# Kernel tuning notes

Measured on AMD Instinct MI355X. Metric: run time of the kernel, lower is better.

## Reference

```python
import jax, jax.numpy as jnp
import numpy as np
import math

N, B, E = 1024, 1, 1024
H = 16
D = E // H
S = 128  # num_samples per row

def setup_inputs() -> dict:
    key = jax.random.key(0)
    ks = jax.random.split(key, 12)
    w = lambda k: jax.random.normal(k, (E, E), jnp.float32) * 0.02
    inp = {
        'query': jax.random.normal(ks[0], (N, B, E), jnp.float32),
        'key':   jax.random.normal(ks[1], (N, B, E), jnp.float32),
        'value': jax.random.normal(ks[2], (N, B, E), jnp.float32),
        'Wq': w(ks[3]), 'bq': jnp.zeros((E,), jnp.float32),
        'Wk': w(ks[4]), 'bk': jnp.zeros((E,), jnp.float32),
        'Wv': w(ks[5]), 'bv': jnp.zeros((E,), jnp.float32),
        'Wo': w(ks[6]), 'bo': jnp.zeros((E,), jnp.float32),
        # per-row sampled column indices, already offset+clamped to [0, N)
        'samples': jax.random.randint(ks[7], (N, S), 0, N, jnp.int32),
    }
    return inp

def reference(query, key, value, Wq, bq, Wk, bk, Wv, bv, Wo, bo, samples):
    n = query.shape[0]
    # projections (torch Linear: x @ W.T + b), split heads -> [B*H, n, D]
    q = (query @ Wq.T + bq).reshape(n, B * H, D).transpose(1, 0, 2)
    k = (key   @ Wk.T + bk).reshape(n, B * H, D).transpose(1, 0, 2)
    v = (value @ Wv.T + bv).reshape(n, B * H, D).transpose(1, 0, 2)
    # emulate per-row unique(): sort, mask duplicates (first occurrence kept)
    cols = jnp.sort(samples, axis=1)                              # [n, S]
    dup = jnp.concatenate([jnp.zeros((n, 1), bool), cols[:, 1:] == cols[:, :-1]], axis=1)
    kg = k[:, cols]                                               # [BH, n, S, D]
    scores = jnp.einsum('hid,hisd->his', q, kg) / jnp.float32(math.sqrt(n))
    scores = jnp.where(dup[None], jnp.float32(-1e30), scores)
    w = jax.nn.softmax(scores, axis=-1)                           # [BH, n, S]
    vg = v[:, cols]                                               # [BH, n, S, D]
    o = jnp.einsum('his,hisd->hid', w, vg)                        # [BH, n, D]
    o = o.transpose(1, 0, 2).reshape(n, B, E)
    return o @ Wo.T + bo
```

## Files before the change

### kernel.cpp

```cpp
#include <hip/hip_runtime.h>
#include <hip/hip_bf16.h>

#define NTOK 1024
#define EMB  1024
#define NH   16
#define HD   64
#define NS   128

typedef unsigned short u16;
typedef unsigned int uint;
typedef __attribute__((ext_vector_type(8))) unsigned short ushort8v;
typedef __attribute__((ext_vector_type(8))) _Float16 half8v;
typedef __attribute__((ext_vector_type(4))) float f32x4;

__device__ __forceinline__ u16 f2h_bits(float f) {
  union { _Float16 h; u16 u; } x; x.h = (_Float16)f; return x.u;
}

__device__ __forceinline__ void gload16(const u16* g, u16* l) {
  __builtin_amdgcn_global_load_lds(
      (const __attribute__((address_space(1))) uint*)g,
      (__attribute__((address_space(3))) uint*)l, 16, 0, 0);
}

__global__ __launch_bounds__(256) void cvt_mask(const float* __restrict__ S0,
                                                const float* __restrict__ S1,
                                                const float* __restrict__ S2,
                                                const float* __restrict__ S3,
                                                const float* __restrict__ S4,
                                                const float* __restrict__ S5,
                                                const float* __restrict__ S6,
                                                const int* __restrict__ samples,
                                                u16* __restrict__ D,
                                                uint* __restrict__ maskg) {
  const int z = blockIdx.y;
  const int t = threadIdx.x;
  if (z == 7) {
    __shared__ uint m[32];
    const int i = blockIdx.x;
    if (t < 32) m[t] = 0u;
    __syncthreads();
    if (t < NS) {
      const int c = samples[(size_t)i * NS + t];
      atomicOr(&m[c >> 5], 1u << (c & 31));
    }
    __syncthreads();
    if (t < 32) maskg[(size_t)i * 32 + t] = m[t];
    return;
  }
  const float* S;
  switch (z) {
    case 0: S = S0; break;
    case 1: S = S1; break;
    case 2: S = S2; break;
    case 3: S = S3; break;
    case 4: S = S4; break;
    case 5: S = S5; break;
    default: S = S6; break;
  }
  const int idx = blockIdx.x * 256 + t;
  const float4 f = ((const float4*)S)[idx];
  ushort4 p;
  p.x = f2h_bits(f.x); p.y = f2h_bits(f.y);
  p.z = f2h_bits(f.z); p.w = f2h_bits(f.w);
  ((ushort4*)(D + ((size_t)z << 20)))[idx] = p;
}

template<bool OUT_F16>
__global__ __launch_bounds__(256) void gemm3(const u16* __restrict__ Ab,
                                             const u16* __restrict__ Bb,
                                             const float* __restrict__ b0,
                                             const float* __restrict__ b1,
                                             const float* __restrict__ b2,
                                             void* __restrict__ Cp) {
  __shared__ u16 buf[2][2][64 * 32];

  const int t = threadIdx.x;
  const int lane = t & 63;
  const int w = t >> 6;
  const int wr = w >> 1, wc = w & 1;
  const int m0 = blockIdx.y * 64;
  const int n0 = blockIdx.x * 64;
  const int z = blockIdx.z;

  const u16* Az = Ab + ((size_t)z << 20);
  const u16* Bz = Bb + ((size_t)z << 20);
  const float* bsel = (z == 0) ? b0 : ((z == 1) ? b1 : b2);

  const int r_abs = w * 16 + (lane >> 2);
  const int schunk = (lane & 3) ^ ((r_abs >> 1) & 3);
  const u16* gA = Az + (size_t)(m0 + r_abs) * 1024 + schunk * 8;
  const u16* gB = Bz + (size_t)(n0 + r_abs) * 1024 + schunk * 8;
  u16* ldsA[2] = { &buf[0][0][(w * 16) * 32], &buf[1][0][(w * 16) * 32] };
  u16* ldsB[2] = { &buf[0][1][(w * 16) * 32], &buf[1][1][(w * 16) * 32] };

  const int fr = lane & 15;
  const int fq = lane >> 4;
  int offA[2], offB[2];
#pragma unroll
  for (int m = 0; m < 2; m++) {
    const int R = wr * 32 + m * 16 + fr;
    offA[m] = R * 32 + (fq ^ ((R >> 1) & 3)) * 8;
  }
#pragma unroll
  for (int n = 0; n < 2; n++) {
    const int R = wc * 32 + n * 16 + fr;
    offB[n] = R * 32 + (fq ^ ((R >> 1) & 3)) * 8;
  }

  f32x4 acc[2][2];
#pragma unroll
  for (int m = 0; m < 2; m++)
#pragma unroll
    for (int n = 0; n < 2; n++) acc[m][n] = (f32x4){0.f, 0.f, 0.f, 0.f};

  gload16(gA, ldsA[0]);
  gload16(gB, ldsB[0]);

  for (int kt = 0; kt < 32; kt++) {
    const int db = kt & 1;
    if (kt < 31) {
      const int k1 = (kt + 1) * 32;
      gload16(gA + k1, ldsA[db ^ 1]);
      gload16(gB + k1, ldsB[db ^ 1]);
      asm volatile("s_waitcnt vmcnt(2)" ::: "memory");
    } else {
      asm volatile("s_waitcnt vmcnt(0)" ::: "memory");
    }
    __builtin_amdgcn_s_barrier();
    __builtin_amdgcn_sched_barrier(0);

    const u16* cA = &buf[db][0][0];
    const u16* cB = &buf[db][1][0];
    half8v a0 = *(const half8v*)&cA[offA[0]];
    half8v a1 = *(const half8v*)&cA[offA[1]];
    half8v bv0 = *(const half8v*)&cB[offB[0]];
    half8v bv1 = *(const half8v*)&cB[offB[1]];
    acc[0][0] = __builtin_amdgcn_mfma_f32_16x16x32_f16(a0, bv0, acc[0][0], 0, 0, 0);
    acc[0][1] = __builtin_amdgcn_mfma_f32_16x16x32_f16(a0, bv1, acc[0][1], 0, 0, 0);
    acc[1][0] = __builtin_amdgcn_mfma_f32_16x16x32_f16(a1, bv0, acc[1][0], 0, 0, 0);
    acc[1][1] = __builtin_amdgcn_mfma_f32_16x16x32_f16(a1, bv1, acc[1][1], 0, 0, 0);

    asm volatile("s_waitcnt lgkmcnt(0)" ::: "memory");
    __builtin_amdgcn_s_barrier();
    __builtin_amdgcn_sched_barrier(0);
  }

  u16*   Cb = (u16*)Cp   + ((size_t)z << 20);
  float* Cf = (float*)Cp + ((size_t)z << 20);

  if (OUT_F16 && z == 2) {
#pragma unroll
    for (int n = 0; n < 2; n++) {
      const int col = n0 + wc * 32 + n * 16 + fr;
      const float bn = bsel[col];
#pragma unroll
      for (int m = 0; m < 2; m++) {
        const int rbase = m0 + wr * 32 + m * 16 + fq * 4;
        ushort4 pk;
        pk.x = f2h_bits(acc[m][n][0] + bn);
        pk.y = f2h_bits(acc[m][n][1] + bn);
        pk.z = f2h_bits(acc[m][n][2] + bn);
        pk.w = f2h_bits(acc[m][n][3] + bn);
        *(ushort4*)&Cb[(size_t)col * 1024 + rbase] = pk;
      }
    }
    return;
  }

#pragma unroll
  for (int n = 0; n < 2; n++) {
    const int col = n0 + wc * 32 + n * 16 + fr;
    const float bn = bsel[col];
#pragma unroll
    for (int m = 0; m < 2; m++) {
      const int rbase = m0 + wr * 32 + m * 16 + fq * 4;
#pragma unroll
      for (int r = 0; r < 4; r++) {
        const float val = acc[m][n][r] + bn;
        if constexpr (OUT_F16)
          Cb[(size_t)(rbase + r) * 1024 + col] = f2h_bits(val);
        else
          Cf[(size_t)(rbase + r) * 1024 + col] = val;
      }
    }
  }
}

__global__ __launch_bounds__(256) void attn7(const u16* __restrict__ Qh,
                                             const u16* __restrict__ Kh,
                                             const u16* __restrict__ Vtg,
                                             const uint* __restrict__ maskg,
                                             u16* __restrict__ O) {
  const int h  = blockIdx.x;
  const int qt = blockIdx.y;
  const int t  = threadIdx.x;
  const int wid = t >> 6;
  const int lane = t & 63;
  const int fr = lane & 15, fq = lane >> 4;

  __shared__ u16 Kl[2][128 * 64];
  __shared__ u16 Vl[2][64 * 128];
  __shared__ u16 Ps[4][16][136];
  __shared__ uint Ms[64][32];

  {
    const uint4* src = (const uint4*)(maskg + (size_t)qt * 64 * 32);
    uint4* dst = (uint4*)Ms;
    dst[t * 2]     = src[t * 2];
    dst[t * 2 + 1] = src[t * 2 + 1];
  }

  half8v qa0, qa1;
  {
    const u16* qp = Qh + (size_t)(qt * 64 + wid * 16 + fr) * EMB + h * HD + fq * 8;
    qa0 = *(const half8v*)qp;
    qa1 = *(const half8v*)(qp + 32);
  }

  const int kRow = wid * 32 + (lane >> 3);
  const int kChO = ((lane & 7) ^ ((lane >> 3) & 7)) * 8;
  const u16* kBase = Kh + h * HD + kChO;
  const int vSub = lane >> 4;
  const int vCh  = lane & 15;
  const u16* vBase = Vtg + (size_t)h * HD * NTOK;

  auto STAGE = [&](int kt_, int b_) {
#pragma unroll
    for (int ii = 0; ii < 4; ii++) {
      const int row = kRow + ii * 8;
      gload16(kBase + (size_t)(kt_ * 128 + row) * EMB,
              &Kl[b_][(wid * 32 + ii * 8) * 64]);
    }
#pragma unroll
    for (int ii = 0; ii < 4; ii++) {
      const int d = wid * 16 + ii * 4 + vSub;
      const int ch = (vCh ^ (d & 15)) * 8;
      gload16(vBase + (size_t)d * NTOK + kt_ * 128 + ch,
              &Vl[b_][(wid * 16 + ii * 4) * 128]);
    }
  };

  f32x4 oacc[4];
#pragma unroll
  for (int ds = 0; ds < 4; ds++) oacc[ds] = (f32x4){0.f, 0.f, 0.f, 0.f};
  float lsum[4] = {0.f, 0.f, 0.f, 0.f};

  STAGE(0, 0);

  for (int kt = 0; kt < 8; kt++) {
    if (kt < 7) {
      STAGE(kt + 1, (kt + 1) & 1);
      asm volatile("s_waitcnt vmcnt(8)" ::: "memory");
    } else {
      asm volatile("s_waitcnt vmcnt(0)" ::: "memory");
    }
    asm volatile("s_waitcnt lgkmcnt(0)" ::: "memory");
    __builtin_amdgcn_s_barrier();
    __builtin_amdgcn_sched_barrier(0);

    const u16* Kc = &Kl[kt & 1][0];
    const u16* Vc = &Vl[kt & 1][0];

    uint4 mq[4];
#pragma unroll
    for (int r = 0; r < 4; r++)
      mq[r] = *(const uint4*)&Ms[wid * 16 + fq * 4 + r][kt * 4];

#pragma unroll
    for (int jb = 0; jb < 8; jb++) {
      f32x4 s = (f32x4){0.f, 0.f, 0.f, 0.f};
      const int R = jb * 16 + fr;
      const half8v b0 = *(const half8v*)&Kc[R * 64 + (fq ^ (fr & 7)) * 8];
      const half8v b1 = *(const half8v*)&Kc[R * 64 + ((4 + fq) ^ (fr & 7)) * 8];
      s = __builtin_amdgcn_mfma_f32_16x16x32_f16(qa0, b0, s, 0, 0, 0);
      s = __builtin_amdgcn_mfma_f32_16x16x32_f16(qa1, b1, s, 0, 0, 0);
#pragma unroll
      for (int r = 0; r < 4; r++) {
        const uint mw = (jb >> 1) == 0 ? mq[r].x
                      : (jb >> 1) == 1 ? mq[r].y
                      : (jb >> 1) == 2 ? mq[r].z : mq[r].w;
        const float p = ((mw >> ((jb & 1) * 16 + fr)) & 1u)
                            ? __expf(s[r] * 0.03125f) : 0.f;
        lsum[r] += p;
        Ps[wid][fq * 4 + r][jb * 16 + fr] = f2h_bits(p);
      }
    }
    asm volatile("s_waitcnt lgkmcnt(0)" ::: "memory");
    __builtin_amdgcn_sched_barrier(0);

#pragma unroll
    for (int jc = 0; jc < 4; jc++) {
      const half8v pa = *(const half8v*)&Ps[wid][fr][jc * 32 + fq * 8];
#pragma unroll
      for (int ds = 0; ds < 4; ds++) {
        const int d = ds * 16 + fr;
        const half8v vb = *(const half8v*)&Vc[d * 128 + ((jc * 4 + fq) ^ fr) * 8];
        oacc[ds] = __builtin_amdgcn_mfma_f32_16x16x32_f16(pa, vb, oacc[ds], 0, 0, 0);
      }
    }
    __builtin_amdgcn_s_barrier();
  }

#pragma unroll
  for (int r = 0; r < 4; r++) {
    float v = lsum[r];
#pragma unroll
    for (int off = 1; off < 16; off <<= 1) v += __shfl_xor(v, off, 16);
    lsum[r] = v;
  }

#pragma unroll
  for (int ds = 0; ds < 4; ds++) {
#pragma unroll
    for (int r = 0; r < 4; r++) {
      O[(size_t)(qt * 64 + wid * 16 + fq * 4 + r) * EMB + h * HD + ds * 16 + fr] =
          f2h_bits(oacc[ds][r] / lsum[r]);
    }
  }
}

extern "C" void kernel_launch(void* const* d_in, const int* in_sizes, int n_in,
                              void* d_out, int out_size, void* d_ws, size_t ws_size,
                              hipStream_t stream) {
  const float* query = (const float*)d_in[0];
  const float* key   = (const float*)d_in[1];
  const float* value = (const float*)d_in[2];
  const float* Wq    = (const float*)d_in[3];
  const float* bq    = (const float*)d_in[4];
  const float* Wk    = (const float*)d_in[5];
  const float* bk    = (const float*)d_in[6];
  const float* Wv    = (const float*)d_in[7];
  const float* bv    = (const float*)d_in[8];
  const float* Wo    = (const float*)d_in[9];
  const float* bo    = (const float*)d_in[10];
  const int* samples = (const int*)d_in[11];
  float* out = (float*)d_out;

  u16* base = (u16*)d_ws;
  u16* Xh = base;
  u16* Wh = base + ((size_t)3 << 20);
  u16* Qh = base + ((size_t)7 << 20);
  u16* Kh = base + ((size_t)8 << 20);
  u16* Vt = base + ((size_t)9 << 20);
  u16* O  = base + ((size_t)10 << 20);
  uint* maskg = (uint*)(base + ((size_t)11 << 20));

  cvt_mask<<<dim3(1024, 8), 256, 0, stream>>>(
      query, key, value, Wq, Wk, Wv, Wo, samples, Xh, maskg);

  gemm3<true><<<dim3(16, 16, 3), 256, 0, stream>>>(Xh, Wh, bq, bk, bv, Qh);

  attn7<<<dim3(NH, 16), 256, 0, stream>>>(Qh, Kh, Vt, maskg, O);

  gemm3<false><<<dim3(16, 16, 1), 256, 0, stream>>>(O, Wh + ((size_t)3 << 20), bo, bo, bo, out);
}
```

Before: 59.03 us.

## Widen QKV projection GEMM tile and transpose score MFMA in attention

```diff
diff --git a/kernel.cpp b/kernel.cpp
--- a/kernel.cpp
+++ b/kernel.cpp
@@ -187,11 +187,131 @@
   }
 }
 
-__global__ __launch_bounds__(256) void attn7(const u16* __restrict__ Qh,
-                                             const u16* __restrict__ Kh,
-                                             const u16* __restrict__ Vtg,
-                                             const uint* __restrict__ maskg,
-                                             u16* __restrict__ O) {
+__global__ __launch_bounds__(256) void gemm3w(const u16* __restrict__ Ab,
+                                              const u16* __restrict__ Bb,
+                                              const float* __restrict__ b0,
+                                              const float* __restrict__ b1,
+                                              const float* __restrict__ b2,
+                                              u16* __restrict__ Cp) {
+  __shared__ u16 As[2][64 * 32];
+  __shared__ u16 Bs[2][128 * 32];
+
+  const int t = threadIdx.x;
+  const int lane = t & 63;
+  const int w = t >> 6;
+  const int wr = w >> 1, wc = w & 1;
+  const int n0 = blockIdx.x * 128;
+  const int m0 = blockIdx.y * 64;
+  const int z = blockIdx.z;
+
+  const u16* Az = Ab + ((size_t)z << 20);
+  const u16* Bz = Bb + ((size_t)z << 20);
+  const float* bsel = (z == 0) ? b0 : ((z == 1) ? b1 : b2);
+
+  const int rA = w * 16 + (lane >> 2);
+  const int cA_ = (lane & 3) ^ ((rA >> 1) & 3);
+  const u16* gA = Az + (size_t)(m0 + rA) * 1024 + cA_ * 8;
+  const int rB0 = w * 32 + (lane >> 2);
+  const int rB1 = rB0 + 16;
+  const int cB0 = (lane & 3) ^ ((rB0 >> 1) & 3);
+  const int cB1 = (lane & 3) ^ ((rB1 >> 1) & 3);
+  const u16* gB0 = Bz + (size_t)(n0 + rB0) * 1024 + cB0 * 8;
+  const u16* gB1 = Bz + (size_t)(n0 + rB1) * 1024 + cB1 * 8;
+
+  const int fr = lane & 15;
+  const int fq = lane >> 4;
+  int offA[2], offB[4];
+#pragma unroll
+  for (int m = 0; m < 2; m++) {
+    const int R = wr * 32 + m * 16 + fr;
+    offA[m] = R * 32 + (fq ^ ((R >> 1) & 3)) * 8;
+  }
+#pragma unroll
+  for (int n = 0; n < 4; n++) {
+    const int R = wc * 64 + n * 16 + fr;
+    offB[n] = R * 32 + (fq ^ ((R >> 1) & 3)) * 8;
+  }
+
+  f32x4 acc[2][4];
+#pragma unroll
+  for (int m = 0; m < 2; m++)
+#pragma unroll
+    for (int n = 0; n < 4; n++) acc[m][n] = (f32x4){0.f, 0.f, 0.f, 0.f};
+
+  gload16(gA,  &As[0][(w * 16) * 32]);
+  gload16(gB0, &Bs[0][(w * 32) * 32]);
+  gload16(gB1, &Bs[0][(w * 32 + 16) * 32]);
+
+  for (int kt = 0; kt < 32; kt++) {
+    const int db = kt & 1;
+    if (kt < 31) {
+      const int k1 = (kt + 1) * 32;
+      gload16(gA + k1,  &As[db ^ 1][(w * 16) * 32]);
+      gload16(gB0 + k1, &Bs[db ^ 1][(w * 32) * 32]);
+      gload16(gB1 + k1, &Bs[db ^ 1][(w * 32 + 16) * 32]);
+      asm volatile("s_waitcnt vmcnt(3)" ::: "memory");
+    } else {
+      asm volatile("s_waitcnt vmcnt(0)" ::: "memory");
+    }
+    __builtin_amdgcn_s_barrier();
+    __builtin_amdgcn_sched_barrier(0);
+
+    half8v a[2], b[4];
+#pragma unroll
+    for (int m = 0; m < 2; m++) a[m] = *(const half8v*)&As[db][offA[m]];
+#pragma unroll
+    for (int n = 0; n < 4; n++) b[n] = *(const half8v*)&Bs[db][offB[n]];
+#pragma unroll
+    for (int m = 0; m < 2; m++)
+#pragma unroll
+      for (int n = 0; n < 4; n++)
+        acc[m][n] = __builtin_amdgcn_mfma_f32_16x16x32_f16(a[m], b[n], acc[m][n], 0, 0, 0);
+
+    asm volatile("s_waitcnt lgkmcnt(0)" ::: "memory");
+    __builtin_amdgcn_s_barrier();
+    __builtin_amdgcn_sched_barrier(0);
+  }
+
+  u16* Cb = Cp + ((size_t)z << 20);
+
+  if (z == 2) {
+#pragma unroll
+    for (int n = 0; n < 4; n++) {
+      const int col = n0 + wc * 64 + n * 16 + fr;
+      const float bn = bsel[col];
+#pragma unroll
+      for (int m = 0; m < 2; m++) {
+        const int rbase = m0 + wr * 32 + m * 16 + fq * 4;
+        ushort4 pk;
+        pk.x = f2h_bits(acc[m][n][0] + bn);
+        pk.y = f2h_bits(acc[m][n][1] + bn);
+        pk.z = f2h_bits(acc[m][n][2] + bn);
+        pk.w = f2h_bits(acc[m][n][3] + bn);
+        *(ushort4*)&Cb[(size_t)col * 1024 + rbase] = pk;
+      }
+    }
+    return;
+  }
+
+#pragma unroll
+  for (int n = 0; n < 4; n++) {
+    const int col = n0 + wc * 64 + n * 16 + fr;
+    const float bn = bsel[col];
+#pragma unroll
+    for (int m = 0; m < 2; m++) {
+      const int rbase = m0 + wr * 32 + m * 16 + fq * 4;
+#pragma unroll
+      for (int r = 0; r < 4; r++)
+        Cb[(size_t)(rbase + r) * 1024 + col] = f2h_bits(acc[m][n][r] + bn);
+    }
+  }
+}
+
+__global__ __launch_bounds__(256) void attn13(const u16* __restrict__ Qh,
+                                              const u16* __restrict__ Kh,
+                                              const u16* __restrict__ Vtg,
+                                              const uint* __restrict__ maskg,
+                                              u16* __restrict__ O) {
   const int h  = blockIdx.x;
   const int qt = blockIdx.y;
   const int t  = threadIdx.x;
@@ -202,13 +322,16 @@
   __shared__ u16 Kl[2][128 * 64];
   __shared__ u16 Vl[2][64 * 128];
   __shared__ u16 Ps[4][16][136];
-  __shared__ uint Ms[64][32];
+  __shared__ uint Ms[64][36];
+  __shared__ float lsums[4][16];
 
   {
     const uint4* src = (const uint4*)(maskg + (size_t)qt * 64 * 32);
-    uint4* dst = (uint4*)Ms;
-    dst[t * 2]     = src[t * 2];
-    dst[t * 2 + 1] = src[t * 2 + 1];
+#pragma unroll
+    for (int j = 0; j < 8; j++) {
+      const int i4 = t + j * 256;
+      *(uint4*)&Ms[i4 >> 3][(i4 & 7) * 4] = src[i4];
+    }
   }
 
   half8v qa0, qa1;
@@ -244,7 +367,7 @@
   f32x4 oacc[4];
 #pragma unroll
   for (int ds = 0; ds < 4; ds++) oacc[ds] = (f32x4){0.f, 0.f, 0.f, 0.f};
-  float lsum[4] = {0.f, 0.f, 0.f, 0.f};
+  float lsum = 0.f;
 
   STAGE(0, 0);
 
@@ -262,10 +385,7 @@
     const u16* Kc = &Kl[kt & 1][0];
     const u16* Vc = &Vl[kt & 1][0];
 
-    uint4 mq[4];
-#pragma unroll
-    for (int r = 0; r < 4; r++)
-      mq[r] = *(const uint4*)&Ms[wid * 16 + fq * 4 + r][kt * 4];
+    const uint4 mq = *(const uint4*)&Ms[wid * 16 + fr][kt * 4];
 
 #pragma unroll
     for (int jb = 0; jb < 8; jb++) {
@@ -273,22 +393,25 @@
       const int R = jb * 16 + fr;
       const half8v b0 = *(const half8v*)&Kc[R * 64 + (fq ^ (fr & 7)) * 8];
       const half8v b1 = *(const half8v*)&Kc[R * 64 + ((4 + fq) ^ (fr & 7)) * 8];
-      s = __builtin_amdgcn_mfma_f32_16x16x32_f16(qa0, b0, s, 0, 0, 0);
-      s = __builtin_amdgcn_mfma_f32_16x16x32_f16(qa1, b1, s, 0, 0, 0);
+      s = __builtin_amdgcn_mfma_f32_16x16x32_f16(b0, qa0, s, 0, 0, 0);
+      s = __builtin_amdgcn_mfma_f32_16x16x32_f16(b1, qa1, s, 0, 0, 0);
+      const uint mw = (jb >> 1) == 0 ? mq.x
+                    : (jb >> 1) == 1 ? mq.y
+                    : (jb >> 1) == 2 ? mq.z : mq.w;
+      const int bb = (jb & 1) * 16 + fq * 4;
+      ushort4 pk;
 #pragma unroll
       for (int r = 0; r < 4; r++) {
-        const uint mw = (jb >> 1) == 0 ? mq[r].x
-                      : (jb >> 1) == 1 ? mq[r].y
-                      : (jb >> 1) == 2 ? mq[r].z : mq[r].w;
-        const float p = ((mw >> ((jb & 1) * 16 + fr)) & 1u)
-                            ? __expf(s[r] * 0.03125f) : 0.f;
-        lsum[r] += p;
-        Ps[wid][fq * 4 + r][jb * 16 + fr] = f2h_bits(p);
+        const float p = ((mw >> (bb + r)) & 1u) ? __expf(s[r] * 0.03125f) : 0.f;
+        lsum += p;
+        ((u16*)&pk)[r] = f2h_bits(p);
       }
+      *(ushort4*)&Ps[wid][fr][jb * 16 + fq * 4] = pk;
     }
     asm volatile("s_waitcnt lgkmcnt(0)" ::: "memory");
     __builtin_amdgcn_sched_barrier(0);
 
+    __builtin_amdgcn_s_setprio(1);
 #pragma unroll
     for (int jc = 0; jc < 4; jc++) {
       const half8v pa = *(const half8v*)&Ps[wid][fr][jc * 32 + fq * 8];
@@ -299,23 +422,26 @@
         oacc[ds] = __builtin_amdgcn_mfma_f32_16x16x32_f16(pa, vb, oacc[ds], 0, 0, 0);
       }
     }
-    __builtin_amdgcn_s_barrier();
-  }
-
-#pragma unroll
-  for (int r = 0; r < 4; r++) {
-    float v = lsum[r];
-#pragma unroll
-    for (int off = 1; off < 16; off <<= 1) v += __shfl_xor(v, off, 16);
-    lsum[r] = v;
-  }
+    __builtin_amdgcn_s_setprio(0);
+    __builtin_amdgcn_s_barrier();
+  }
+
+  lsum += __shfl_xor(lsum, 16, 64);
+  lsum += __shfl_xor(lsum, 32, 64);
+  if (fq == 0) lsums[wid][fr] = lsum;
+  asm volatile("s_waitcnt lgkmcnt(0)" ::: "memory");
+  __builtin_amdgcn_sched_barrier(0);
+
+  float ls[4];
+#pragma unroll
+  for (int r = 0; r < 4; r++) ls[r] = lsums[wid][fq * 4 + r];
 
 #pragma unroll
   for (int ds = 0; ds < 4; ds++) {
 #pragma unroll
     for (int r = 0; r < 4; r++) {
       O[(size_t)(qt * 64 + wid * 16 + fq * 4 + r) * EMB + h * HD + ds * 16 + fr] =
-          f2h_bits(oacc[ds][r] / lsum[r]);
+          f2h_bits(oacc[ds][r] / ls[r]);
     }
   }
 }
@@ -349,9 +475,9 @@
   cvt_mask<<<dim3(1024, 8), 256, 0, stream>>>(
       query, key, value, Wq, Wk, Wv, Wo, samples, Xh, maskg);
 
-  gemm3<true><<<dim3(16, 16, 3), 256, 0, stream>>>(Xh, Wh, bq, bk, bv, Qh);
-
-  attn7<<<dim3(NH, 16), 256, 0, stream>>>(Qh, Kh, Vt, maskg, O);
+  gemm3w<<<dim3(8, 16, 3), 256, 0, stream>>>(Xh, Wh, bq, bk, bv, Qh);
+
+  attn13<<<dim3(NH, 16), 256, 0, stream>>>(Qh, Kh, Vt, maskg, O);
 
   gemm3<false><<<dim3(16, 16, 1), 256, 0, stream>>>(O, Wh + ((size_t)3 << 20), bo, bo, bo, out);
 }
```

Result: slower. 63.49 us (+7.6%).

## Split attention key tiles across two waves per query group with LDS reduction

Applied to the files above, without the earlier changes.

```diff
diff --git a/kernel.cpp b/kernel.cpp
--- a/kernel.cpp
+++ b/kernel.cpp
@@ -187,39 +187,41 @@
   }
 }
 
-__global__ __launch_bounds__(256) void attn7(const u16* __restrict__ Qh,
-                                             const u16* __restrict__ Kh,
-                                             const u16* __restrict__ Vtg,
-                                             const uint* __restrict__ maskg,
-                                             u16* __restrict__ O) {
+__global__ __launch_bounds__(512) void attn14(const u16* __restrict__ Qh,
+                                              const u16* __restrict__ Kh,
+                                              const u16* __restrict__ Vtg,
+                                              const uint* __restrict__ maskg,
+                                              u16* __restrict__ O) {
   const int h  = blockIdx.x;
   const int qt = blockIdx.y;
   const int t  = threadIdx.x;
   const int wid = t >> 6;
+  const int qg  = wid >> 1;
+  const int kh  = wid & 1;
   const int lane = t & 63;
   const int fr = lane & 15, fq = lane >> 4;
 
   __shared__ u16 Kl[2][128 * 64];
   __shared__ u16 Vl[2][64 * 128];
-  __shared__ u16 Ps[4][16][136];
-  __shared__ uint Ms[64][32];
+  __shared__ u16 Ps[8][16][72];
+  __shared__ uint Ms[64][36];
+  __shared__ float Obuf[4][16][64];
+  __shared__ float Lbuf[4][16];
 
   {
     const uint4* src = (const uint4*)(maskg + (size_t)qt * 64 * 32);
-    uint4* dst = (uint4*)Ms;
-    dst[t * 2]     = src[t * 2];
-    dst[t * 2 + 1] = src[t * 2 + 1];
+    *(uint4*)&Ms[t >> 3][(t & 7) * 4] = src[t];
   }
 
   half8v qa0, qa1;
   {
-    const u16* qp = Qh + (size_t)(qt * 64 + wid * 16 + fr) * EMB + h * HD + fq * 8;
+    const u16* qp = Qh + (size_t)(qt * 64 + qg * 16 + fr) * EMB + h * HD + fq * 8;
     qa0 = *(const half8v*)qp;
     qa1 = *(const half8v*)(qp + 32);
   }
 
-  const int kRow = wid * 32 + (lane >> 3);
-  const int kChO = ((lane & 7) ^ ((lane >> 3) & 7)) * 8;
+  const int kR3 = lane >> 3;
+  const int kChO = ((lane & 7) ^ (kR3 & 7)) * 8;
   const u16* kBase = Kh + h * HD + kChO;
   const int vSub = lane >> 4;
   const int vCh  = lane & 15;
@@ -227,17 +229,17 @@
 
   auto STAGE = [&](int kt_, int b_) {
 #pragma unroll
-    for (int ii = 0; ii < 4; ii++) {
-      const int row = kRow + ii * 8;
+    for (int ii = 0; ii < 2; ii++) {
+      const int row = wid * 16 + ii * 8 + kR3;
       gload16(kBase + (size_t)(kt_ * 128 + row) * EMB,
-              &Kl[b_][(wid * 32 + ii * 8) * 64]);
-    }
-#pragma unroll
-    for (int ii = 0; ii < 4; ii++) {
-      const int d = wid * 16 + ii * 4 + vSub;
+              &Kl[b_][(wid * 16 + ii * 8) * 64]);
+    }
+#pragma unroll
+    for (int ii = 0; ii < 2; ii++) {
+      const int d = wid * 8 + ii * 4 + vSub;
       const int ch = (vCh ^ (d & 15)) * 8;
       gload16(vBase + (size_t)d * NTOK + kt_ * 128 + ch,
-              &Vl[b_][(wid * 16 + ii * 4) * 128]);
+              &Vl[b_][(wid * 8 + ii * 4) * 128]);
     }
   };
 
@@ -251,7 +253,7 @@
   for (int kt = 0; kt < 8; kt++) {
     if (kt < 7) {
       STAGE(kt + 1, (kt + 1) & 1);
-      asm volatile("s_waitcnt vmcnt(8)" ::: "memory");
+      asm volatile("s_waitcnt vmcnt(4)" ::: "memory");
     } else {
       asm volatile("s_waitcnt vmcnt(0)" ::: "memory");
     }
@@ -262,24 +264,22 @@
     const u16* Kc = &Kl[kt & 1][0];
     const u16* Vc = &Vl[kt & 1][0];
 
-    uint4 mq[4];
+    uint2 mq[4];
 #pragma unroll
     for (int r = 0; r < 4; r++)
-      mq[r] = *(const uint4*)&Ms[wid * 16 + fq * 4 + r][kt * 4];
-
-#pragma unroll
-    for (int jb = 0; jb < 8; jb++) {
+      mq[r] = *(const uint2*)&Ms[qg * 16 + fq * 4 + r][kt * 4 + kh * 2];
+
+#pragma unroll
+    for (int jb = 0; jb < 4; jb++) {
       f32x4 s = (f32x4){0.f, 0.f, 0.f, 0.f};
-      const int R = jb * 16 + fr;
+      const int R = kh * 64 + jb * 16 + fr;
       const half8v b0 = *(const half8v*)&Kc[R * 64 + (fq ^ (fr & 7)) * 8];
       const half8v b1 = *(const half8v*)&Kc[R * 64 + ((4 + fq) ^ (fr & 7)) * 8];
       s = __builtin_amdgcn_mfma_f32_16x16x32_f16(qa0, b0, s, 0, 0, 0);
       s = __builtin_amdgcn_mfma_f32_16x16x32_f16(qa1, b1, s, 0, 0, 0);
 #pragma unroll
       for (int r = 0; r < 4; r++) {
-        const uint mw = (jb >> 1) == 0 ? mq[r].x
-                      : (jb >> 1) == 1 ? mq[r].y
-                      : (jb >> 1) == 2 ? mq[r].z : mq[r].w;
+        const uint mw = (jb >> 1) ? mq[r].y : mq[r].x;
         const float p = ((mw >> ((jb & 1) * 16 + fr)) & 1u)
                             ? __expf(s[r] * 0.03125f) : 0.f;
         lsum[r] += p;
@@ -289,16 +289,19 @@
     asm volatile("s_waitcnt lgkmcnt(0)" ::: "memory");
     __builtin_amdgcn_sched_barrier(0);
 
-#pragma unroll
-    for (int jc = 0; jc < 4; jc++) {
+    __builtin_amdgcn_s_setprio(1);
+#pragma unroll
+    for (int jc = 0; jc < 2; jc++) {
       const half8v pa = *(const half8v*)&Ps[wid][fr][jc * 32 + fq * 8];
 #pragma unroll
       for (int ds = 0; ds < 4; ds++) {
         const int d = ds * 16 + fr;
-        const half8v vb = *(const half8v*)&Vc[d * 128 + ((jc * 4 + fq) ^ fr) * 8];
+        const half8v vb =
+            *(const half8v*)&Vc[d * 128 + ((kh * 8 + jc * 4 + fq) ^ fr) * 8];
         oacc[ds] = __builtin_amdgcn_mfma_f32_16x16x32_f16(pa, vb, oacc[ds], 0, 0, 0);
       }
     }
+    __builtin_amdgcn_s_setprio(0);
     __builtin_amdgcn_s_barrier();
   }
 
@@ -310,12 +313,30 @@
     lsum[r] = v;
   }
 
-#pragma unroll
-  for (int ds = 0; ds < 4; ds++) {
-#pragma unroll
-    for (int r = 0; r < 4; r++) {
-      O[(size_t)(qt * 64 + wid * 16 + fq * 4 + r) * EMB + h * HD + ds * 16 + fr] =
-          f2h_bits(oacc[ds][r] / lsum[r]);
+  if (kh == 1) {
+#pragma unroll
+    for (int ds = 0; ds < 4; ds++)
+#pragma unroll
+      for (int r = 0; r < 4; r++)
+        Obuf[qg][fq * 4 + r][ds * 16 + fr] = oacc[ds][r];
+    if (fr == 0) {
+#pragma unroll
+      for (int r = 0; r < 4; r++) Lbuf[qg][fq * 4 + r] = lsum[r];
+    }
+  }
+  __syncthreads();
+  if (kh == 0) {
+    float ls[4];
+#pragma unroll
+    for (int r = 0; r < 4; r++) ls[r] = lsum[r] + Lbuf[qg][fq * 4 + r];
+#pragma unroll
+    for (int ds = 0; ds < 4; ds++) {
+#pragma unroll
+      for (int r = 0; r < 4; r++) {
+        const float v = oacc[ds][r] + Obuf[qg][fq * 4 + r][ds * 16 + fr];
+        O[(size_t)(qt * 64 + qg * 16 + fq * 4 + r) * EMB + h * HD + ds * 16 + fr] =
+            f2h_bits(v / ls[r]);
+      }
     }
   }
 }
@@ -351,7 +372,7 @@
 
   gemm3<true><<<dim3(16, 16, 3), 256, 0, stream>>>(Xh, Wh, bq, bk, bv, Qh);
 
-  attn7<<<dim3(NH, 16), 256, 0, stream>>>(Qh, Kh, Vt, maskg, O);
+  attn14<<<dim3(NH, 16), 512, 0, stream>>>(Qh, Kh, Vt, maskg, O);
 
   gemm3<false><<<dim3(16, 16, 1), 256, 0, stream>>>(O, Wh + ((size_t)3 << 20), bo, bo, bo, out);
 }
```

Result: faster. 57.20 us (-3.1%).
